# Kernel optimization log

Measured on AMD Instinct MI355X. Metric: run time of the kernel, lower is better.

The kernel has to match this reference:

```python
import jax, jax.numpy as jnp
import numpy as np

B, T, K, H = 8, 1024, 128, 8
TOP_K = 64
KS = 5  # conv kernel size for Q/K
DN = ('NCH', 'OIH', 'NCH')


def setup_inputs() -> dict:
    key = jax.random.key(0)
    ks = jax.random.split(key, 9)
    s = 0.05
    return {
        'x': jax.random.normal(ks[0], (B, T, K), jnp.float32),
        'Wq': jax.random.normal(ks[1], (K * H, K, KS), jnp.float32) * s,
        'bq': jax.random.normal(ks[2], (K * H,), jnp.float32) * s,
        'Wk': jax.random.normal(ks[3], (K * H, K, KS), jnp.float32) * s,
        'bk': jax.random.normal(ks[4], (K * H,), jnp.float32) * s,
        'Wv': jax.random.normal(ks[5], (K * H, K, 1), jnp.float32) * s,
        'bv': jax.random.normal(ks[6], (K * H,), jnp.float32) * s,
        'Wu': jax.random.normal(ks[7], (K, K * H), jnp.float32) * s,
        'bu': jax.random.normal(ks[8], (K,), jnp.float32) * s,
    }


def _prep(z, b, k, h, t, scale):
    # z: (b, k*h, t) conv output; torch view(b,k,h,t) then transposes -> (b,h,t,k)
    z = z.reshape(b, k, h, t)
    z = jnp.transpose(z, (0, 2, 3, 1)) * scale  # (b, h, t, k)
    # torch: transpose(1,2).contiguous().view(b*h, t, k) -- replicate exactly
    z = jnp.transpose(z, (0, 2, 1, 3)).reshape(b * h, t, k)
    return z


def reference(x, Wq, bq, Wk, bk, Wv, bv, Wu, bu):
    b, t, k = x.shape
    h = H
    xc = jnp.transpose(x, (0, 2, 1))  # (b, k, t)
    # causal left-pad KS-1 for Q/K convs; V is pointwise (kernel 1)
    q = jax.lax.conv_general_dilated(xc, Wq, (1,), [(KS - 1, 0)], dimension_numbers=DN) + bq[None, :, None]
    kk = jax.lax.conv_general_dilated(xc, Wk, (1,), [(KS - 1, 0)], dimension_numbers=DN) + bk[None, :, None]
    v = jax.lax.conv_general_dilated(xc, Wv, (1,), [(0, 0)], dimension_numbers=DN) + bv[None, :, None]
    scale = k ** -0.25
    q = _prep(q, b, k, h, t, scale)
    kk = _prep(kk, b, k, h, t, scale)
    v = _prep(v, b, k, h, t, 1.0)
    w = jnp.einsum('btk,bsk->bts', q, kk)  # (b*h, t, t)
    # top-k sparsification: keep entries >= k-th largest per row, else row min
    largest, _ = jax.lax.top_k(w, TOP_K)
    thresh = jnp.min(largest, axis=-1, keepdims=True)
    row_min = jnp.min(w, axis=-1, keepdims=True)
    w = jnp.where(w >= thresh, w, row_min)
    # causal mask (strict upper triangle -> -inf)
    causal = jnp.triu(jnp.ones((t, t), bool), 1)
    w = jnp.where(causal[None], -jnp.inf, w)
    w = jax.nn.softmax(w, axis=-1)
    out = jnp.einsum('bts,bsk->btk', w, v)  # (b*h, t, k)
    out = out.reshape(b, h, t, k)
    out = jnp.transpose(out, (0, 2, 1, 3)).reshape(b, t, k * h)
    return out @ Wu.T + bu
```

## Files before the change

kernel.cpp:

```cpp
#include <hip/hip_runtime.h>
#include <hip/hip_fp16.h>
#include <cstdint>

using f16 = _Float16;
typedef __attribute__((ext_vector_type(8))) _Float16 f16x8;
typedef __attribute__((ext_vector_type(4))) _Float16 f16x4;
typedef __attribute__((ext_vector_type(4))) float f32x4;

#define MFMA16(a, b, c) __builtin_amdgcn_mfma_f32_16x16x32_f16((a), (b), (c), 0, 0, 0)

__device__ __forceinline__ f16x8 ldfrag(const f16* p) { return *(const f16x8*)p; }

__device__ __forceinline__ void dma16(const f16* g, f16* l) {
  __builtin_amdgcn_global_load_lds(
      (const __attribute__((address_space(1))) void*)g,
      (__attribute__((address_space(3))) void*)l, 16, 0, 0);
}
__device__ __forceinline__ void wait_vm0() {
  asm volatile("s_waitcnt vmcnt(0)" ::: "memory");
}
__device__ __forceinline__ void wait_lgkm0() {
  asm volatile("s_waitcnt lgkmcnt(0)" ::: "memory");
}
__device__ __forceinline__ void wait_vm4() {
  asm volatile("s_waitcnt vmcnt(4)" ::: "memory");
}

static const int64_t NX = 1048576;
static const int64_t NW = 655360;
static const int64_t NV = 131072;

__global__ __launch_bounds__(256) void k0_prep(
    const float* __restrict__ x, const float* __restrict__ Wq,
    const float* __restrict__ Wk, const float* __restrict__ Wv,
    const float* __restrict__ Wu,
    f16* __restrict__ xh, f16* __restrict__ xl,
    f16* __restrict__ Wqh, f16* __restrict__ Wql,
    f16* __restrict__ Wkh, f16* __restrict__ Wkl,
    f16* __restrict__ Wvb, f16* __restrict__ Wub) {
  int64_t i = (int64_t)blockIdx.x * 256 + threadIdx.x;
  if (i < NX) {
    const float v = x[i];
    const f16 h = (f16)v;
    xh[i] = h; xl[i] = (f16)(v - (float)h);
  } else if (i < NX + NW) {
    int64_t d = i - NX;
    int j = (int)(d >> 17);
    int rem = (int)(d & 131071);
    int o = rem >> 7, c = rem & 127;
    const float v = Wq[(int64_t)(o * 128 + c) * 5 + j];
    const f16 h = (f16)v;
    Wqh[d] = h; Wql[d] = (f16)(v - (float)h);
  } else if (i < NX + 2 * NW) {
    int64_t d = i - NX - NW;
    int j = (int)(d >> 17);
    int rem = (int)(d & 131071);
    int o = rem >> 7, c = rem & 127;
    const float v = Wk[(int64_t)(o * 128 + c) * 5 + j];
    const f16 h = (f16)v;
    Wkh[d] = h; Wkl[d] = (f16)(v - (float)h);
  } else if (i < NX + 2 * NW + NV) {
    int64_t d = i - NX - 2 * NW;
    Wvb[d] = (f16)Wv[d];
  } else {
    int64_t d = i - NX - 2 * NW - NV;
    Wub[d] = (f16)Wu[d];
  }
}

#define STAGE_QK(DST, PASS, VALEXPR)                                    \
  {                                                                     \
    __syncthreads();                                                    \
    _Pragma("unroll")                                                   \
    for (int nt = 0; nt < 8; ++nt) {                                    \
      const int o = o0 + nt * 16 + lo;                                  \
      const int kcl = (o >> 3) & 63, hh = o & 7;                        \
      _Pragma("unroll")                                                 \
      for (int rtl = 0; rtl < 2; ++rtl) {                               \
        const int rt = (PASS) * 2 + rtl;                                \
        _Pragma("unroll")                                               \
        for (int r = 0; r < 4; ++r) {                                   \
          const int t2l = (rtl * 16 + quad * 4 + r) * 8 + hh;           \
          lds[t2l * 72 + kcl] = (VALEXPR);                              \
        }                                                               \
      }                                                                 \
    }                                                                   \
    __syncthreads();                                                    \
    _Pragma("unroll")                                                   \
    for (int p = 0; p < 8; ++p) {                                       \
      const int idx = p * 256 + tid;                                    \
      const int a = idx >> 3, c8 = (idx & 7) * 8;                       \
      *(f16x8*)(DST + ((int64_t)m * 1024 + t2b + (PASS) * 256 + a) * 128 + \
                half * 64 + c8) = *(const f16x8*)&lds[a * 72 + c8];     \
    }                                                                   \
  }

__global__ __launch_bounds__(256) void k1_conv(
    const f16* __restrict__ xh, const f16* __restrict__ xl,
    const f16* __restrict__ Wqh, const f16* __restrict__ Wql,
    const f16* __restrict__ Wkh, const f16* __restrict__ Wkl,
    const f16* __restrict__ Wvb,
    const float* __restrict__ bq, const float* __restrict__ bk,
    const float* __restrict__ bv,
    f16* __restrict__ q3h, f16* __restrict__ q3l,
    f16* __restrict__ k3h, f16* __restrict__ k3l,
    f16* __restrict__ v3T) {
  __shared__ f16 shm[36384];
  f16* const wbuf = shm;
  f16* const xbuf = shm + 18432;
  f16* const lds  = shm;
  const int tid = threadIdx.x;
  const int w = tid >> 6, lane = tid & 63;
  const int quad = lane >> 4, lo = lane & 15;
  const int r0 = blockIdx.x * 64;
  const int bb = r0 >> 10;
  const int m  = r0 >> 7;
  const int t2b = (r0 & 127) * 8;
  const int tloc = r0 & 1023;
  const int half = blockIdx.y;
  const int isK = blockIdx.z;
  const int o0 = half * 512 + w * 128;

  const f16* Wh = isK ? Wkh : Wqh;
  const f16* Wl = isK ? Wkl : Wql;
  const float* bias = isK ? bk : bq;

#pragma unroll
  for (int p = 0; p < 9; ++p) {
    const int u = p * 256 + tid;
    if (u < 2176) {
      const int row = u >> 5, tz = (u >> 4) & 1, c8 = (u & 15) * 8;
      int lt = tloc - 4 + row;
      if (lt < 0) lt = 0;
      const f16* src = (tz ? xl : xh) + ((int64_t)(bb * 1024 + lt)) * 128 + c8;
      *(f16x8*)&xbuf[row * 264 + tz * 128 + c8] = *(const f16x8*)src;
    }
  }
  __syncthreads();

  const int64_t wlane = (int64_t)(lane & 15) * 128 + (lane >> 4) * 8;

  if (!isK) {
    f32x4 av[4][8];
#pragma unroll
    for (int rt = 0; rt < 4; ++rt)
#pragma unroll
      for (int i = 0; i < 8; ++i)
#pragma unroll
        for (int r = 0; r < 4; ++r) av[rt][i][r] = 0.f;

#pragma unroll
    for (int g = 0; g < 4; ++g) {
#pragma unroll
      for (int s = 0; s < 2; ++s) {
        const int64_t vsrc = (int64_t)(o0 + (g * 2 + s) * 16) * 128 + wlane;
#pragma unroll
        for (int kk = 0; kk < 4; ++kk)
          dma16(Wvb + vsrc + kk * 32, wbuf + w * 4096 + s * 2048 + kk * 512);
      }
      wait_vm0();
#pragma unroll
      for (int kk = 0; kk < 4; ++kk) {
        f16x8 a[4];
#pragma unroll
        for (int rt = 0; rt < 4; ++rt)
          a[rt] = *(const f16x8*)&xbuf[(rt * 16 + lo + 4) * 264 + kk * 32 +
                                       quad * 8];
#pragma unroll
        for (int s = 0; s < 2; ++s) {
          const f16x8 bv8 = *(const f16x8*)&wbuf[w * 4096 + s * 2048 + kk * 512 +
                                                 quad * 128 + lo * 8];
#pragma unroll
          for (int rt = 0; rt < 4; ++rt)
            av[rt][g * 2 + s] = MFMA16(a[rt], bv8, av[rt][g * 2 + s]);
        }
      }
      wait_lgkm0();
    }
    __syncthreads();
#pragma unroll
    for (int pass = 0; pass < 2; ++pass) {
#pragma unroll
      for (int nt = 0; nt < 8; ++nt) {
        const int o = o0 + nt * 16 + lo;
        const float vbv = bv[o];
        const int kcl = (o >> 3) & 63, hh = o & 7;
#pragma unroll
        for (int rtl = 0; rtl < 2; ++rtl)
#pragma unroll
          for (int r = 0; r < 4; ++r) {
            const int t2l = (rtl * 16 + quad * 4 + r) * 8 + hh;
            lds[kcl * 264 + t2l] = (f16)(av[pass * 2 + rtl][nt][r] + vbv);
          }
      }
      __syncthreads();
#pragma unroll
      for (int p = 0; p < 8; ++p) {
        const int idx = p * 256 + tid;
        const int kcl = idx >> 5, t8 = (idx & 31) * 8;
        *(f16x8*)(v3T + ((int64_t)m * 128 + half * 64 + kcl) * 1024 + t2b +
                  pass * 256 + t8) = *(const f16x8*)&lds[kcl * 264 + t8];
      }
      __syncthreads();
    }
  }

  f32x4 aq[4][8];
#pragma unroll
  for (int rt = 0; rt < 4; ++rt)
#pragma unroll
    for (int i = 0; i < 8; ++i)
#pragma unroll
      for (int r = 0; r < 4; ++r) { aq[rt][i][r] = 0.f; }

  for (int j = 0; j < 5; ++j) {
    const bool z0 = (tloc == 0);
#pragma unroll
    for (int nt = 0; nt < 8; ++nt) {
      const int64_t wsrc =
          (int64_t)j * 131072 + (int64_t)(o0 + nt * 16) * 128 + wlane;
#pragma unroll
      for (int kk = 0; kk < 4; ++kk) {
        dma16(Wh + wsrc + kk * 32, wbuf + w * 4096 + kk * 512);
        dma16(Wl + wsrc + kk * 32, wbuf + w * 4096 + 2048 + kk * 512);
      }
      wait_vm4();
#pragma unroll
      for (int kk = 0; kk < 4; ++kk) {
        if (kk == 2) wait_vm0();
        const f16x8 bh =
            *(const f16x8*)&wbuf[w * 4096 + kk * 512 + quad * 128 + lo * 8];
        const f16x8 bl =
            *(const f16x8*)&wbuf[w * 4096 + 2048 + kk * 512 + quad * 128 + lo * 8];
#pragma unroll
        for (int rt = 0; rt < 4; ++rt) {
          f16x8 ah = *(const f16x8*)&xbuf[(rt * 16 + lo + j) * 264 + kk * 32 +
                                          quad * 8];
          f16x8 al = *(const f16x8*)&xbuf[(rt * 16 + lo + j) * 264 + 128 +
                                          kk * 32 + quad * 8];
          if (rt == 0 && z0 && (lo + j < 4)) {
#pragma unroll
            for (int e = 0; e < 8; ++e) { ah[e] = (f16)0; al[e] = (f16)0; }
          }
          aq[rt][nt] = MFMA16(ah, bh, aq[rt][nt]);
          aq[rt][nt] = MFMA16(ah, bl, aq[rt][nt]);
          aq[rt][nt] = MFMA16(al, bh, aq[rt][nt]);
        }
      }
      wait_lgkm0();
    }
  }

  const float SC = 0.29730177875068026f;
#pragma unroll
  for (int nt = 0; nt < 8; ++nt) {
    const int o = o0 + nt * 16 + lo;
    const float vb = bias[o];
#pragma unroll
    for (int rt = 0; rt < 4; ++rt)
#pragma unroll
      for (int r = 0; r < 4; ++r) aq[rt][nt][r] = (aq[rt][nt][r] + vb) * SC;
  }

  if (!isK) {
    STAGE_QK(q3h, 0, (f16)aq[rt][nt][r])
    STAGE_QK(q3h, 1, (f16)aq[rt][nt][r])
    STAGE_QK(q3l, 0, (f16)(aq[rt][nt][r] - (float)(f16)aq[rt][nt][r]))
    STAGE_QK(q3l, 1, (f16)(aq[rt][nt][r] - (float)(f16)aq[rt][nt][r]))
  } else {
    STAGE_QK(k3h, 0, (f16)aq[rt][nt][r])
    STAGE_QK(k3h, 1, (f16)aq[rt][nt][r])
    STAGE_QK(k3l, 0, (f16)(aq[rt][nt][r] - (float)(f16)aq[rt][nt][r]))
    STAGE_QK(k3l, 1, (f16)(aq[rt][nt][r] - (float)(f16)aq[rt][nt][r]))
  }
}

__global__ __launch_bounds__(512, 4) void k234_attn(
    const f16* __restrict__ q3h, const f16* __restrict__ q3l,
    const f16* __restrict__ k3h, const f16* __restrict__ k3l,
    const f16* __restrict__ v3T, f16* __restrict__ A) {
  __shared__ float Sb[16 * 516];
  __shared__ f16 kbuf[16384];
  const int tid = threadIdx.x;
  const int w = tid >> 6, lane = tid & 63;
  const int quad = lane >> 4, lo = lane & 15;
  const int qd = lane & 3, cit = lane >> 2;
  const int hid = blockIdx.y * 64 + blockIdx.x;
  const int m = (hid & 7) * 8 + ((hid >> 3) >> 6);
  const int r0 = ((hid >> 3) & 63) * 16;

  const int64_t qoff = ((int64_t)m * 1024 + r0 + lo) * 128;
  f16x8 qh[4], ql[4];
#pragma unroll
  for (int kk = 0; kk < 4; ++kk) {
    qh[kk] = ldfrag(q3h + qoff + kk * 32 + quad * 8);
    ql[kk] = ldfrag(q3l + qoff + kk * 32 + quad * 8);
  }

  unsigned key[2][16];
  unsigned kmn0 = 0xFFFFFFFFu, kmn1 = 0xFFFFFFFFu;

#pragma unroll
  for (int half = 0; half < 2; ++half) {
    f32x4 acc[4];
#pragma unroll
    for (int i = 0; i < 4; ++i)
#pragma unroll
      for (int r = 0; r < 4; ++r) acc[i][r] = 0.f;

    for (int kp = 0; kp < 2; ++kp) {
#pragma unroll
      for (int cc = 0; cc < 4; ++cc) {
        const int c0 = half * 512 + cc * 128;
        const int64_t rowg = (int64_t)(m * 1024 + c0 + w * 16 + cit) * 128;
#pragma unroll
        for (int t = 0; t < 2; ++t) {
          const f16* srcb = t ? k3l : k3h;
#pragma unroll
          for (int kkh = 0; kkh < 2; ++kkh)
            dma16(srcb + rowg + (kp * 2 + kkh) * 32 + qd * 8,
                  kbuf + (w * 4 + t * 2 + kkh) * 512);
        }
        wait_vm0();
#pragma unroll
        for (int kkh = 0; kkh < 2; ++kkh) {
          const int kkg = kp * 2 + kkh;
          f16x8 bh = *(const f16x8*)(kbuf + (w * 4 + kkh) * 512 +
                                     (lo * 4 + quad) * 8);
          f16x8 bl = *(const f16x8*)(kbuf + (w * 4 + 2 + kkh) * 512 +
                                     (lo * 4 + quad) * 8);
          acc[cc] = MFMA16(qh[kkg], bh, acc[cc]);
          acc[cc] = MFMA16(qh[kkg], bl, acc[cc]);
          acc[cc] = MFMA16(ql[kkg], bh, acc[cc]);
        }
        wait_lgkm0();
      }
    }
#pragma unroll
    for (int cc = 0; cc < 4; ++cc)
#pragma unroll
      for (int r = 0; r < 4; ++r)
        Sb[(quad * 4 + r) * 516 + cc * 128 + w * 16 + lo] = acc[cc][r];
    __syncthreads();
#pragma unroll
    for (int rr = 0; rr < 2; ++rr) {
      const float4* rp = (const float4*)(Sb + (w * 2 + rr) * 516);
#pragma unroll
      for (int i2 = 0; i2 < 2; ++i2) {
        const float4 f4 = rp[i2 * 64 + lane];
        const float fe[4] = {f4.x, f4.y, f4.z, f4.w};
#pragma unroll
        for (int e = 0; e < 4; ++e) {
          const unsigned u = __builtin_bit_cast(unsigned, fe[e]);
          const unsigned k = (u & 0x80000000u) ? ~u : (u | 0x80000000u);
          key[rr][half * 8 + i2 * 4 + e] = k;
          if (rr == 0) kmn0 = min(kmn0, k); else kmn1 = min(kmn1, k);
        }
      }
    }
    __syncthreads();
  }

  f16* P16 = (f16*)Sb;
  {
#pragma unroll
    for (int off = 32; off; off >>= 1) {
      kmn0 = min(kmn0, (unsigned)__shfl_xor((int)kmn0, off));
      kmn1 = min(kmn1, (unsigned)__shfl_xor((int)kmn1, off));
    }
    unsigned th0 = 0u, th1 = 0u;
    for (int b = 31; b >= 0; --b) {
      const unsigned c0 = th0 | (1u << b);
      const unsigned c1 = th1 | (1u << b);
      int cnt0 = 0, cnt1 = 0;
#pragma unroll
      for (int i = 0; i < 16; ++i) {
        cnt0 += (int)__popcll(__ballot(key[0][i] >= c0));
        cnt1 += (int)__popcll(__ballot(key[1][i] >= c1));
      }
      if (cnt0 >= 64) th0 = c0;
      if (cnt1 >= 64) th1 = c1;
    }

#pragma unroll
    for (int rr = 0; rr < 2; ++rr) {
      const unsigned kth = rr ? th1 : th0;
      const unsigned kmn = rr ? kmn1 : kmn0;
      const int row = w * 2 + rr, t2 = r0 + row;
      const unsigned umn = (kmn & 0x80000000u) ? (kmn ^ 0x80000000u) : ~kmn;
      const float mn = __builtin_bit_cast(float, umn);
      const unsigned ukv = (kth & 0x80000000u) ? (kth ^ 0x80000000u) : ~kth;
      const float kv = __builtin_bit_cast(float, ukv);

      float ev[16];
      float sum = 0.f;
#pragma unroll
      for (int j = 0; j < 16; ++j) {
        const int s = (j >> 3) * 512 + ((j >> 2) & 1) * 256 + lane * 4 + (j & 3);
        const unsigned k = key[rr][j];
        const unsigned uu = (k & 0x80000000u) ? (k ^ 0x80000000u) : ~k;
        const float f = __builtin_bit_cast(float, uu);
        const float ww = (k >= kth) ? f : mn;
        const float x = (s <= t2) ? __expf(ww - kv) : 0.f;
        ev[j] = x;
        sum += x;
      }
      for (int off = 32; off; off >>= 1) sum += __shfl_xor(sum, off);
      const float inv = 1.0f / sum;

      f16* prow = P16 + row * 1032;
#pragma unroll
      for (int hh = 0; hh < 2; ++hh)
#pragma unroll
        for (int i2 = 0; i2 < 2; ++i2) {
          f16x4 pk;
#pragma unroll
          for (int e = 0; e < 4; ++e)
            pk[e] = (f16)(ev[hh * 8 + i2 * 4 + e] * inv);
          *(f16x4*)(prow + hh * 512 + i2 * 256 + lane * 4) = pk;
        }
    }
  }
  __syncthreads();

  {
    f32x4 oa0, oa1;
#pragma unroll
    for (int r = 0; r < 4; ++r) { oa0[r] = 0.f; oa1[r] = 0.f; }
    const int64_t vrow = (int64_t)(m * 128 + w * 16 + cit) * 1024;
    const int nkb = (r0 >> 6) + 1;
    for (int kb = 0; kb < nkb; ++kb) {
#pragma unroll
      for (int kkh = 0; kkh < 2; ++kkh)
        dma16(v3T + vrow + kb * 64 + kkh * 32 + qd * 8,
              kbuf + (w * 2 + kkh) * 512);
      wait_vm0();
      {
        const f16x8 vf0 = *(const f16x8*)(kbuf + (w * 2) * 512 +
                                          (lo * 4 + quad) * 8);
        const f16x8 vf1 = *(const f16x8*)(kbuf + (w * 2 + 1) * 512 +
                                          (lo * 4 + quad) * 8);
        const f16x8 af0 = *(const f16x8*)(P16 + lo * 1032 + kb * 64 + quad * 8);
        const f16x8 af1 =
            *(const f16x8*)(P16 + lo * 1032 + kb * 64 + 32 + quad * 8);
        oa0 = MFMA16(af0, vf0, oa0);
        oa1 = MFMA16(af1, vf1, oa1);
      }
      wait_lgkm0();
    }
#pragma unroll
    for (int r = 0; r < 4; ++r)
      A[((int64_t)m * 1024 + r0 + quad * 4 + r) * 128 + w * 16 + lo] =
          (f16)(oa0[r] + oa1[r]);
  }
}

__global__ __launch_bounds__(256) void k5_proj(
    const f16* __restrict__ A, const f16* __restrict__ Wub,
    const float* __restrict__ bu, float* __restrict__ out) {
  const int w = threadIdx.x >> 6, lane = threadIdx.x & 63;
  const int quad = lane >> 4, lo = lane & 15;
  const int rt = w & 1, ch = w >> 1;
  const int r0 = blockIdx.x * 32 + rt * 16;
  const int r = r0 + lo;
  const int bI = r >> 10, t2 = r & 1023;

  f32x4 acc[4];
#pragma unroll
  for (int i = 0; i < 4; ++i)
#pragma unroll
    for (int rr = 0; rr < 4; ++rr) acc[i][rr] = 0.f;

#pragma unroll 2
  for (int kk = 0; kk < 32; ++kk) {
    const int o = kk * 32 + quad * 8;
    const int j = o >> 7, kc = o & 127;
    f16x8 a = ldfrag(A + (((int64_t)(bI * 8 + j) * 1024 + t2) * 128 + kc));
    f16x8 wb[4];
#pragma unroll
    for (int nt = 0; nt < 4; ++nt)
      wb[nt] = ldfrag(Wub + (int64_t)(ch * 64 + nt * 16 + lo) * 1024 + o);
#pragma unroll
    for (int nt = 0; nt < 4; ++nt) acc[nt] = MFMA16(a, wb[nt], acc[nt]);
  }
#pragma unroll
  for (int nt = 0; nt < 4; ++nt) {
    const int col = ch * 64 + nt * 16 + lo;
    const float bias = bu[col];
#pragma unroll
    for (int rr = 0; rr < 4; ++rr) {
      const int row = r0 + quad * 4 + rr;
      out[(int64_t)row * 128 + col] = acc[nt][rr] + bias;
    }
  }
}

extern "C" void kernel_launch(void* const* d_in, const int* in_sizes, int n_in,
                              void* d_out, int out_size, void* d_ws, size_t ws_size,
                              hipStream_t stream) {
  const float* x  = (const float*)d_in[0];
  const float* Wq = (const float*)d_in[1];
  const float* bq = (const float*)d_in[2];
  const float* Wk = (const float*)d_in[3];
  const float* bk = (const float*)d_in[4];
  const float* Wv = (const float*)d_in[5];
  const float* bv = (const float*)d_in[6];
  const float* Wu = (const float*)d_in[7];
  const float* bu = (const float*)d_in[8];
  float* out = (float*)d_out;

  char* ws = (char*)d_ws;
  f16* xh  = (f16*)ws;  ws += 2097152;
  f16* xl  = (f16*)ws;  ws += 2097152;
  f16* Wqh = (f16*)ws;  ws += 1310720;
  f16* Wql = (f16*)ws;  ws += 1310720;
  f16* Wkh = (f16*)ws;  ws += 1310720;
  f16* Wkl = (f16*)ws;  ws += 1310720;
  f16* Wvb = (f16*)ws;  ws += 262144;
  f16* Wub = (f16*)ws;  ws += 262144;
  f16* q3h = (f16*)ws;  ws += 16777216;
  f16* q3l = (f16*)ws;  ws += 16777216;
  f16* k3h = (f16*)ws;  ws += 16777216;
  f16* k3l = (f16*)ws;  ws += 16777216;
  f16* v3T = (f16*)ws;  ws += 16777216;
  f16* A   = (f16*)ws;  ws += 16777216;

  k0_prep<<<10240, 256, 0, stream>>>(x, Wq, Wk, Wv, Wu,
                                     xh, xl, Wqh, Wql, Wkh, Wkl, Wvb, Wub);

  k1_conv<<<dim3(128, 2, 2), 256, 0, stream>>>(xh, xl, Wqh, Wql, Wkh, Wkl, Wvb,
                                               bq, bk, bv, q3h, q3l, k3h, k3l,
                                               v3T);

  k234_attn<<<dim3(64, 64), 512, 0, stream>>>(q3h, q3l, k3h, k3l, v3T, A);

  k5_proj<<<256, 256, 0, stream>>>(A, Wub, bu, out);

  (void)in_sizes; (void)n_in; (void)out_size; (void)ws_size;
}
```

Measured before the change: 445.0 us.

## Double-buffer V tile DMA and prefetch first tiles before softmax phase

Issues the first two V tile loads into LDS before the top-k threshold and softmax phase, then double-buffers the V loads in the PV loop using a partial vmcnt wait. This hides global load latency behind compute. The lane-to-row mapping for the DMA is also changed (qd/cit swapped) so each lane reads its fragment contiguously from LDS at lane*8. The cost is more LDS buffer slots per wave and an early reuse of kbuf, which must not clash with the softmax phase.

```diff
diff --git a/kernel.cpp b/kernel.cpp
--- a/kernel.cpp
+++ b/kernel.cpp
@@ -24,6 +24,9 @@
 }
 __device__ __forceinline__ void wait_vm4() {
   asm volatile("s_waitcnt vmcnt(4)" ::: "memory");
+}
+__device__ __forceinline__ void wait_vm2() {
+  asm volatile("s_waitcnt vmcnt(2)" ::: "memory");
 }
 
 static const int64_t NX = 1048576;
@@ -284,7 +287,7 @@
   const int tid = threadIdx.x;
   const int w = tid >> 6, lane = tid & 63;
   const int quad = lane >> 4, lo = lane & 15;
-  const int qd = lane & 3, cit = lane >> 2;
+  const int qd = lane >> 4, cit = lane & 15;
   const int hid = blockIdx.y * 64 + blockIdx.x;
   const int m = (hid & 7) * 8 + ((hid >> 3) >> 6);
   const int r0 = ((hid >> 3) & 63) * 16;
@@ -325,10 +328,8 @@
 #pragma unroll
         for (int kkh = 0; kkh < 2; ++kkh) {
           const int kkg = kp * 2 + kkh;
-          f16x8 bh = *(const f16x8*)(kbuf + (w * 4 + kkh) * 512 +
-                                     (lo * 4 + quad) * 8);
-          f16x8 bl = *(const f16x8*)(kbuf + (w * 4 + 2 + kkh) * 512 +
-                                     (lo * 4 + quad) * 8);
+          f16x8 bh = *(const f16x8*)(kbuf + (w * 4 + kkh) * 512 + lane * 8);
+          f16x8 bl = *(const f16x8*)(kbuf + (w * 4 + 2 + kkh) * 512 + lane * 8);
           acc[cc] = MFMA16(qh[kkg], bh, acc[cc]);
           acc[cc] = MFMA16(qh[kkg], bl, acc[cc]);
           acc[cc] = MFMA16(ql[kkg], bh, acc[cc]);
@@ -360,6 +361,18 @@
     }
     __syncthreads();
   }
+
+  const int64_t vrow = (int64_t)(m * 128 + w * 16 + cit) * 1024;
+  const int nkb = (r0 >> 6) + 1;
+#define VISSUE(KB, PAIR)                                                 \
+  {                                                                      \
+    dma16(v3T + vrow + (KB) * 64 + qd * 8,                               \
+          kbuf + (w * 4 + (PAIR) * 2) * 512);                            \
+    dma16(v3T + vrow + (KB) * 64 + 32 + qd * 8,                          \
+          kbuf + (w * 4 + (PAIR) * 2 + 1) * 512);                        \
+  }
+  VISSUE(0, 0)
+  if (nkb > 1) VISSUE(1, 1)
 
   f16* P16 = (f16*)Sb;
   {
@@ -427,19 +440,15 @@
     f32x4 oa0, oa1;
 #pragma unroll
     for (int r = 0; r < 4; ++r) { oa0[r] = 0.f; oa1[r] = 0.f; }
-    const int64_t vrow = (int64_t)(m * 128 + w * 16 + cit) * 1024;
-    const int nkb = (r0 >> 6) + 1;
     for (int kb = 0; kb < nkb; ++kb) {
-#pragma unroll
-      for (int kkh = 0; kkh < 2; ++kkh)
-        dma16(v3T + vrow + kb * 64 + kkh * 32 + qd * 8,
-              kbuf + (w * 2 + kkh) * 512);
-      wait_vm0();
+      if (kb + 1 < nkb) wait_vm2();
+      else wait_vm0();
+      const int pair = kb & 1;
       {
-        const f16x8 vf0 = *(const f16x8*)(kbuf + (w * 2) * 512 +
-                                          (lo * 4 + quad) * 8);
-        const f16x8 vf1 = *(const f16x8*)(kbuf + (w * 2 + 1) * 512 +
-                                          (lo * 4 + quad) * 8);
+        const f16x8 vf0 = *(const f16x8*)(kbuf + (w * 4 + pair * 2) * 512 +
+                                          lane * 8);
+        const f16x8 vf1 = *(const f16x8*)(kbuf + (w * 4 + pair * 2 + 1) * 512 +
+                                          lane * 8);
         const f16x8 af0 = *(const f16x8*)(P16 + lo * 1032 + kb * 64 + quad * 8);
         const f16x8 af1 =
             *(const f16x8*)(P16 + lo * 1032 + kb * 64 + 32 + quad * 8);
@@ -447,7 +456,9 @@
         oa1 = MFMA16(af1, vf1, oa1);
       }
       wait_lgkm0();
-    }
+      if (kb + 2 < nkb) VISSUE(kb + 2, pair)
+    }
+#undef VISSUE
 #pragma unroll
     for (int r = 0; r < 4; ++r)
       A[((int64_t)m * 1024 + r0 + quad * 4 + r) * 128 + w * 16 + lo] =
```

Measured after the change: 587.6 us. 32.1% more time.
